# Kernel optimization log

Measured on AMD Instinct MI355X. Metric: run time of the kernel, lower is better.

The kernel has to match this reference:

```python
import jax, jax.numpy as jnp
import numpy as np

# Model dims (from init_kwargs): T=12, dx=4, du=2 -> D = T*(dx+du) = 72
T, DX, DU = 12, 4, 2
D = T * (DX + DU)          # flow_dim = 72
MID = D // 2               # mid-split mask: first MID features transformed
CTX = 2 * DX               # context = cat(start, goal) = 8
HID = 64                   # ResidualNet / MLP hidden size
NBLK = 16                  # number of (LULinear, Coupling) blocks
B = 65536


def setup_inputs() -> dict:
    key = jax.random.key(0)
    ks = jax.random.split(key, 16)
    n = lambda k, s, sc=1.0: sc * jax.random.normal(k, s, dtype=jnp.float32)
    inp = {
        "trajectories": n(ks[0], (B, T, DX + DU)),
        "start": n(ks[1], (B, DX)),
        "goal": n(ks[2], (B, DX)),
        # LULinear params per block: strictly-lower / strictly-upper entries,
        # unconstrained diag (softplus(0.5413)~=1 -> near-identity init), bias
        "lu_lower": n(ks[3], (NBLK, D, D), 0.01),
        "lu_upper": n(ks[4], (NBLK, D, D), 0.01),
        "lu_diag": 0.5413 + n(ks[5], (NBLK, D), 0.01),
        "lu_bias": n(ks[6], (NBLK, D), 0.01),
        # Coupling conditioner ResidualNet (in=MID+CTX, hidden=64, 2 blocks, out=2*MID)
        "cn_W0": n(ks[7], (NBLK, HID, MID + CTX), 0.05),
        "cn_b0": jnp.zeros((NBLK, HID), jnp.float32),
        "cn_ctxW": n(ks[8], (NBLK, 2, HID, CTX), 0.1),
        "cn_ctxb": jnp.zeros((NBLK, 2, HID), jnp.float32),
        "cn_l1W": n(ks[9], (NBLK, 2, HID, HID), 0.1),
        "cn_l1b": jnp.zeros((NBLK, 2, HID), jnp.float32),
        "cn_l2W": n(ks[10], (NBLK, 2, HID, HID), 0.1),
        "cn_l2b": jnp.zeros((NBLK, 2, HID), jnp.float32),
        "cn_Wf": n(ks[11], (NBLK, D, HID), 0.05),
        "cn_bf": jnp.zeros((NBLK, D), jnp.float32),
        # ConditionalDiagonalNormal context encoder MLP: ctx -> 2*D
        "enc_W1": n(ks[12], (HID, CTX), 0.1),
        "enc_b1": jnp.zeros((HID,), jnp.float32),
        "enc_W2": n(ks[13], (2 * D, HID), 0.05),
        "enc_b2": jnp.zeros((2 * D,), jnp.float32),
    }
    return inp


def reference(trajectories, start, goal, lu_lower, lu_upper, lu_diag, lu_bias,
              cn_W0, cn_b0, cn_ctxW, cn_ctxb, cn_l1W, cn_l1b, cn_l2W, cn_l2b,
              cn_Wf, cn_bf, enc_W1, enc_b1, enc_W2, enc_b2):
    Bn = trajectories.shape[0]
    x = trajectories.reshape(Bn, D)
    ctx = jnp.concatenate([start, goal], axis=1)  # [B, CTX]
    eye = jnp.eye(D, dtype=x.dtype)

    def resnet(h, W0, b0, cW, cb, l1W, l1b, l2W, l2b, Wf, bf):
        # nflows ResidualNet: initial layer on cat(inputs, context), 2 residual
        # blocks with GLU context gating, final linear.
        t = jnp.concatenate([h, ctx], axis=1) @ W0.T + b0
        for i in range(2):
            a = jax.nn.relu(t) @ l1W[i].T + l1b[i]
            a = jax.nn.relu(a) @ l2W[i].T + l2b[i]
            t = t + a * jax.nn.sigmoid(ctx @ cW[i].T + cb[i])  # GLU
        return t @ Wf.T + bf

    def body(carry, p):
        x, ld = carry
        lL, lU, ldg, lb, W0, b0, cW, cb, l1W, l1b, l2W, l2b, Wf, bf = p
        # LULinear: W = L @ U, L unit lower-tri, U upper-tri, diag = softplus + eps
        diag = jax.nn.softplus(ldg) + 1e-3
        W = (jnp.tril(lL, -1) + eye) @ (jnp.triu(lU, 1) + jnp.diag(diag))
        x = x @ W.T + lb
        ld = ld + jnp.sum(jnp.log(diag))
        # Affine coupling, mid-split: first MID transformed, last MID identity
        h_id = x[:, MID:]
        params = resnet(h_id, W0, b0, cW, cb, l1W, l1b, l2W, l2b, Wf, bf)
        shift = params[:, :MID]
        scale = jax.nn.sigmoid(params[:, MID:] + 2.0) + 1e-3
        x = jnp.concatenate([x[:, :MID] * scale + shift, h_id], axis=1)
        ld = ld + jnp.sum(jnp.log(scale), axis=1)
        return (x, ld), None

    stacked = (lu_lower, lu_upper, lu_diag, lu_bias, cn_W0, cn_b0, cn_ctxW,
               cn_ctxb, cn_l1W, cn_l1b, cn_l2W, cn_l2b, cn_Wf, cn_bf)
    (noise, logdet), _ = jax.lax.scan(body, (x, jnp.zeros((Bn,), x.dtype)), stacked)

    # ConditionalDiagonalNormal base: encoder MLP ctx -> (means, log_stds)
    h = jax.nn.relu(ctx @ enc_W1.T + enc_b1)
    p = h @ enc_W2.T + enc_b2
    means, log_std = p[:, :D], p[:, D:]
    z = (noise - means) * jnp.exp(-log_std)
    base_lp = (-0.5 * jnp.sum(z * z, axis=1) - jnp.sum(log_std, axis=1)
               - 0.5 * D * jnp.log(2.0 * jnp.pi))
    return base_lp + logdet
```

## Files before the change

kernel.cpp:

```cpp
#include <hip/hip_runtime.h>
#include <math.h>

#define DD   72
#define MID  36
#define NBLK 16

typedef _Float16 half8 __attribute__((ext_vector_type(8)));
typedef _Float16 half4 __attribute__((ext_vector_type(4)));
typedef float    f32x4 __attribute__((ext_vector_type(4)));

#define PB    37376
#define S1O   0
#define S2O   7680
#define RBO   11776
#define RB_L1 0
#define RB_L2 4096
#define RB_GW 8192
#define S4O   32256
#define E1O   (16 * PB)
#define E2O   (E1O + 2048)

__device__ inline half4 pk4(f32x4 v) {
    half4 h; h[0] = (_Float16)v[0]; h[1] = (_Float16)v[1];
    h[2] = (_Float16)v[2]; h[3] = (_Float16)v[3]; return h;
}
__device__ inline half4 pk4r(f32x4 v) {
    half4 h;
    h[0] = (_Float16)fmaxf(v[0], 0.f); h[1] = (_Float16)fmaxf(v[1], 0.f);
    h[2] = (_Float16)fmaxf(v[2], 0.f); h[3] = (_Float16)fmaxf(v[3], 0.f);
    return h;
}
__device__ inline float sigf(float x) {
    return __fdividef(1.f, 1.f + __expf(-x));
}
__device__ inline f32x4 MF(half8 a, half8 b, f32x4 c) {
    return __builtin_amdgcn_mfma_f32_16x16x32_f16(a, b, c, 0, 0, 0);
}

__global__ __launch_bounds__(256) void prep_all(
    const float* __restrict__ lu_lower, const float* __restrict__ lu_upper,
    const float* __restrict__ lu_diag,  const float* __restrict__ lu_bias,
    const float* __restrict__ cn_W0, const float* __restrict__ cn_ctxW,
    const float* __restrict__ cn_l1W, const float* __restrict__ cn_l2W,
    const float* __restrict__ cn_Wf, const float* __restrict__ enc_W1,
    const float* __restrict__ enc_W2,
    const float* __restrict__ cn_b0, const float* __restrict__ cn_ctxb,
    const float* __restrict__ enc_b1,
    _Float16* __restrict__ AR, float* __restrict__ wsLd)
{
    const int tid = threadIdx.x;
    __shared__ float Ls[DD][DD + 1];
    __shared__ float Us[DD][DD + 1];
    __shared__ float diag[DD], ldp[DD];

    if (blockIdx.x < 80) {
        const int wg  = blockIdx.x;
        const int blk = wg / 5, mt = wg % 5;
        const float* L = lu_lower + blk * DD * DD;
        const float* U = lu_upper + blk * DD * DD;
        for (int e = tid; e < DD * DD; e += 256) {
            Ls[e / DD][e % DD] = L[e];
            Us[e / DD][e % DD] = U[e];
        }
        if (tid < DD) {
            float v  = lu_diag[blk * DD + tid];
            float sp = log1pf(expf(v)) + 0.001f;
            diag[tid] = sp; ldp[tid] = logf(sp);
        }
        __syncthreads();
        if (mt == 0 && tid == 0) {
            float s = 0.f;
            for (int i = 0; i < DD; ++i) s += ldp[i];
            wsLd[blk] = s;
        }
        if (tid < 192) {
            const int kt = tid >> 6, lane = tid & 63;
            const int m  = mt * 16 + (lane & 15);
            const int k0 = kt * 32 + (lane >> 4) * 8;
            float acc[8] = {0.f,0.f,0.f,0.f,0.f,0.f,0.f,0.f};
            if (m < DD) {
                for (int kk = 0; kk < m; ++kk) {
                    const float a = Ls[m][kk];
                    #pragma unroll
                    for (int j = 0; j < 8; ++j) {
                        const int k = k0 + j;
                        if (k < DD && kk < k) acc[j] = fmaf(a, Us[kk][k], acc[j]);
                    }
                }
                #pragma unroll
                for (int j = 0; j < 8; ++j) {
                    const int k = k0 + j;
                    if (k < DD) {
                        if      (m < k)  acc[j] += Us[m][k];
                        else if (m == k) acc[j] += diag[k];
                        else             acc[j] += Ls[m][k] * diag[k];
                    }
                }
            }
            half8 hv;
            #pragma unroll
            for (int j = 0; j < 8; ++j) {
                const int k = k0 + j;
                float v = 0.f;
                if (m < DD) {
                    if      (k < DD)  v = acc[j];
                    else if (k == DD) v = lu_bias[blk * DD + m];
                }
                hv[j] = (_Float16)v;
            }
            *(half8*)(AR + (size_t)blk * PB + S1O + (size_t)(mt * 3 + kt) * 512
                      + (size_t)lane * 8) = hv;
        }
        return;
    }

    int gid = (blockIdx.x - 80) * 256 + tid;
    int fid = gid >> 6, lane = gid & 63;
    if (fid >= 950) return;
    const int mrow = lane & 15, kcol0 = (lane >> 4) * 8;

    const float* src = nullptr; const float* bias = nullptr;
    size_t dst = 0;
    int m = 0, kbase = 0, rows = 64, kv_lo = 0, kv_hi = 64, sstr = 64, ksub = 0, kbias = -1;

    if (fid < 128) {
        int blk = fid >> 3, f = fid & 7;
        int mt = f >> 1, kt = f & 1;
        src = cn_W0 + (size_t)blk * 64 * 44; sstr = 44;
        dst = (size_t)blk * PB + S2O + (size_t)f * 512;
        m = mt * 16 + mrow; kbase = kt * 32 + kcol0; kv_hi = 44;
        bias = cn_b0 + (size_t)blk * 64; kbias = 44;
    } else if (fid < 384) {
        int id = fid - 128, bi = id >> 3, f = id & 7;
        int mt = f >> 1, kt = f & 1;
        src = cn_l1W + (size_t)bi * 4096;
        dst = (size_t)(bi >> 1) * PB + RBO + (size_t)(bi & 1) * 10240 + RB_L1 + (size_t)f * 512;
        m = mt * 16 + mrow; kbase = kt * 32 + kcol0;
    } else if (fid < 640) {
        int id = fid - 384, bi = id >> 3, f = id & 7;
        int mt = f >> 1, kt = f & 1;
        src = cn_l2W + (size_t)bi * 4096;
        dst = (size_t)(bi >> 1) * PB + RBO + (size_t)(bi & 1) * 10240 + RB_L2 + (size_t)f * 512;
        m = mt * 16 + mrow; kbase = kt * 32 + kcol0;
    } else if (fid < 768) {
        int id = fid - 640, bi = id >> 2, mt = id & 3;
        src = cn_ctxW + (size_t)bi * 512; sstr = 8;
        dst = (size_t)(bi >> 1) * PB + RBO + (size_t)(bi & 1) * 10240 + RB_GW + (size_t)mt * 512;
        m = mt * 16 + mrow; kbase = 32 + kcol0; kv_lo = 36; kv_hi = 44; ksub = 36;
        bias = cn_ctxb + (size_t)bi * 64; kbias = 44;
    } else if (fid < 928) {
        int id = fid - 768, blk = id / 10, f = id % 10;
        int mt = f >> 1, kt = f & 1;
        src = cn_Wf + (size_t)blk * 4608;
        dst = (size_t)blk * PB + S4O + (size_t)f * 512;
        m = mt * 16 + mrow; kbase = kt * 32 + kcol0; rows = 72;
    } else if (fid < 932) {
        int mt = fid - 928;
        src = enc_W1; sstr = 8;
        dst = E1O + (size_t)mt * 512;
        m = mt * 16 + mrow; kbase = 32 + kcol0; kv_lo = 36; kv_hi = 44; ksub = 36;
        bias = enc_b1; kbias = 44;
    } else {
        int id = fid - 932, mt = id >> 1, kt = id & 1;
        src = enc_W2;
        dst = E2O + (size_t)id * 512;
        m = mt * 16 + mrow; kbase = kt * 32 + kcol0; rows = 144;
    }
    half8 hv;
    #pragma unroll
    for (int j = 0; j < 8; ++j) {
        const int k = kbase + j;
        float v = 0.f;
        if (m < rows) {
            if (k >= kv_lo && k < kv_hi) v = src[(size_t)m * sstr + (k - ksub)];
            else if (k == kbias)         v = bias[m];
        }
        hv[j] = (_Float16)v;
    }
    *(half8*)(AR + dst + (size_t)lane * 8) = hv;
}

#define LDH8(off) (*(const half8*)(AR + (size_t)(off) + lane8))
#define MFMA_A(acc, off, bf) acc = MF(LDH8(off), bf, acc)

__global__ __launch_bounds__(256, 4) void flow_kernel(
    const float* __restrict__ traj,
    const float* __restrict__ start,
    const float* __restrict__ goal,
    const float* __restrict__ cn_l1b,
    const float* __restrict__ cn_l2b,
    const float* __restrict__ cn_bf,
    const float* __restrict__ enc_b2,
    const _Float16* __restrict__ AR,
    const float* __restrict__ wsLd,
    float* __restrict__ out, int B)
{
    __shared__ __align__(16) _Float16 ActX[64 * 104];
    __shared__ __align__(16) _Float16 ActH[64 * 72];
    __shared__ __align__(16) _Float16 ActT[64 * 72];

    const int tid  = threadIdx.x;
    const int lane = tid & 63;
    const int w    = __builtin_amdgcn_readfirstlane(tid >> 6);
    const int n    = lane & 15, lg = lane >> 4;
    const int bg0  = blockIdx.x * 64;
    const size_t lane8 = (size_t)lane * 8;

    #pragma unroll
    for (int r = 0; r < 9; ++r) {
        int e = tid + 256 * r;
        int b = e / 36, p = e % 36;
        float2 v = *(const float2*)(traj + (size_t)(bg0 + b) * DD + 2 * p);
        ActX[b * 104 + 2 * p]     = (_Float16)v.x;
        ActX[b * 104 + 2 * p + 1] = (_Float16)v.y;
    }
    #pragma unroll
    for (int r = 0; r < 8; ++r) {
        int e = tid + 256 * r;
        int b = e / 32, c = 72 + e % 32;
        ActX[b * 104 + c] = (c == 72) ? (_Float16)1.f : (_Float16)0.f;
    }
    {
        int b = tid >> 2, cp = tid & 3;
        const float* s = (cp < 2) ? (start + (size_t)(bg0 + b) * 4 + 2 * cp)
                                  : (goal  + (size_t)(bg0 + b) * 4 + 2 * (cp - 2));
        ActH[b * 72 + 36 + 2 * cp]     = (_Float16)s[0];
        ActH[b * 72 + 36 + 2 * cp + 1] = (_Float16)s[1];
    }
    #pragma unroll
    for (int r = 0; r < 7; ++r) {
        int e = tid + 256 * r;
        int b = e / 28, c = 44 + e % 28;
        ActH[b * 72 + c] = (c == 44) ? (_Float16)1.f : (_Float16)0.f;
    }

    half8 s1p0 = LDH8(S1O + 0 * 512), s1p1 = LDH8(S1O + 1 * 512),
          s1p2 = LDH8(S1O + 2 * 512), s1p3 = LDH8(S1O + 3 * 512),
          s1p4 = LDH8(S1O + 4 * 512), s1p5 = LDH8(S1O + 5 * 512);

    __syncthreads();

    const int bx = (16 * w + n) * 104;
    const int bh = (16 * w + n) * 72;
    const int bt = (16 * w + n) * 72;

    float ld_acc = 0.f;
    const f32x4 z4 = {0.f, 0.f, 0.f, 0.f};

    #pragma unroll 1
    for (int blk = 0; blk < NBLK; ++blk) {
        __syncthreads();
        const size_t B0 = (size_t)blk * PB;

        half8 f6  = LDH8(B0 + S1O + 6 * 512),  f7  = LDH8(B0 + S1O + 7 * 512),
              f8  = LDH8(B0 + S1O + 8 * 512),  f9  = LDH8(B0 + S1O + 9 * 512),
              f10 = LDH8(B0 + S1O + 10 * 512), f11 = LDH8(B0 + S1O + 11 * 512),
              f12 = LDH8(B0 + S1O + 12 * 512), f13 = LDH8(B0 + S1O + 13 * 512),
              f14 = LDH8(B0 + S1O + 14 * 512);
        half8 bx0 = *(const half8*)&ActX[bx + 0  + lg * 8];
        half8 bx1 = *(const half8*)&ActX[bx + 32 + lg * 8];
        half8 bx2 = *(const half8*)&ActX[bx + 64 + lg * 8];
        f32x4 y[5];
        y[0] = MF(s1p2, bx2, MF(s1p1, bx1, MF(s1p0, bx0, z4)));
        y[1] = MF(s1p5, bx2, MF(s1p4, bx1, MF(s1p3, bx0, z4)));
        y[2] = MF(f8,  bx2, MF(f7,  bx1, MF(f6,  bx0, z4)));
        y[3] = MF(f11, bx2, MF(f10, bx1, MF(f9,  bx0, z4)));
        y[4] = MF(f14, bx2, MF(f13, bx1, MF(f12, bx0, z4)));

        half8 g0 = LDH8(B0 + S2O + 0 * 512), g1 = LDH8(B0 + S2O + 1 * 512),
              g2 = LDH8(B0 + S2O + 2 * 512), g3 = LDH8(B0 + S2O + 3 * 512),
              g4 = LDH8(B0 + S2O + 4 * 512), g5 = LDH8(B0 + S2O + 5 * 512),
              g6 = LDH8(B0 + S2O + 6 * 512), g7 = LDH8(B0 + S2O + 7 * 512);
        if (lg >= 1) { half4 hv = pk4(y[2]); int m0 = 32 + lg * 4;
            *(half4*)&ActX[bx + m0] = hv; *(half4*)&ActH[bh + m0 - 36] = hv; }
        {            half4 hv = pk4(y[3]); int m0 = 48 + lg * 4;
            *(half4*)&ActX[bx + m0] = hv; *(half4*)&ActH[bh + m0 - 36] = hv; }
        if (lg < 2) { half4 hv = pk4(y[4]); int m0 = 64 + lg * 4;
            *(half4*)&ActX[bx + m0] = hv; *(half4*)&ActH[bh + m0 - 36] = hv; }
        half8 bh0 = *(const half8*)&ActH[bh + 0  + lg * 8];
        half8 bh1 = *(const half8*)&ActH[bh + 32 + lg * 8];
        f32x4 t[4];
        t[0] = MF(g1, bh1, MF(g0, bh0, z4));
        t[1] = MF(g3, bh1, MF(g2, bh0, z4));
        t[2] = MF(g5, bh1, MF(g4, bh0, z4));
        t[3] = MF(g7, bh1, MF(g6, bh0, z4));

        #pragma unroll
        for (int i = 0; i < 2; ++i) {
            const size_t RB = B0 + RBO + (size_t)i * 10240;
            half8 r0 = LDH8(RB + RB_L1 + 0 * 512), r1 = LDH8(RB + RB_L1 + 1 * 512),
                  r2 = LDH8(RB + RB_L1 + 2 * 512), r3 = LDH8(RB + RB_L1 + 3 * 512),
                  r4 = LDH8(RB + RB_L1 + 4 * 512), r5 = LDH8(RB + RB_L1 + 5 * 512),
                  r6 = LDH8(RB + RB_L1 + 6 * 512), r7 = LDH8(RB + RB_L1 + 7 * 512);
            #pragma unroll
            for (int mt = 0; mt < 4; ++mt)
                *(half4*)&ActT[bt + mt * 16 + lg * 4] = pk4r(t[mt]);
            half8 bt0 = *(const half8*)&ActT[bt + 0  + lg * 8];
            half8 bt1 = *(const half8*)&ActT[bt + 32 + lg * 8];
            f32x4 a1[4];
            a1[0] = MF(r1, bt1, MF(r0, bt0, z4));
            a1[1] = MF(r3, bt1, MF(r2, bt0, z4));
            a1[2] = MF(r5, bt1, MF(r4, bt0, z4));
            a1[3] = MF(r7, bt1, MF(r6, bt0, z4));
            half8 q0 = LDH8(RB + RB_L2 + 0 * 512), q1 = LDH8(RB + RB_L2 + 1 * 512),
                  q2 = LDH8(RB + RB_L2 + 2 * 512), q3 = LDH8(RB + RB_L2 + 3 * 512),
                  q4 = LDH8(RB + RB_L2 + 4 * 512), q5 = LDH8(RB + RB_L2 + 5 * 512),
                  q6 = LDH8(RB + RB_L2 + 6 * 512), q7 = LDH8(RB + RB_L2 + 7 * 512);
            half8 w0 = LDH8(RB + RB_GW + 0 * 512), w1 = LDH8(RB + RB_GW + 1 * 512),
                  w2 = LDH8(RB + RB_GW + 2 * 512), w3 = LDH8(RB + RB_GW + 3 * 512);
            #pragma unroll
            for (int mt = 0; mt < 4; ++mt) {
                const float4 bb = *(const float4*)(cn_l1b + (blk * 2 + i) * 64 + mt * 16 + lg * 4);
                a1[mt][0] += bb.x; a1[mt][1] += bb.y; a1[mt][2] += bb.z; a1[mt][3] += bb.w;
                *(half4*)&ActT[bt + mt * 16 + lg * 4] = pk4r(a1[mt]);
            }
            bt0 = *(const half8*)&ActT[bt + 0  + lg * 8];
            bt1 = *(const half8*)&ActT[bt + 32 + lg * 8];
            f32x4 a2[4], gg[4];
            a2[0] = MF(q1, bt1, MF(q0, bt0, z4));
            a2[1] = MF(q3, bt1, MF(q2, bt0, z4));
            a2[2] = MF(q5, bt1, MF(q4, bt0, z4));
            a2[3] = MF(q7, bt1, MF(q6, bt0, z4));
            gg[0] = MF(w0, bh1, z4); gg[1] = MF(w1, bh1, z4);
            gg[2] = MF(w2, bh1, z4); gg[3] = MF(w3, bh1, z4);
            #pragma unroll
            for (int mt = 0; mt < 4; ++mt) {
                const float4 b2 = *(const float4*)(cn_l2b + (blk * 2 + i) * 64 + mt * 16 + lg * 4);
                #pragma unroll
                for (int r = 0; r < 4; ++r) {
                    float av = a2[mt][r] + ((const float*)&b2)[r];
                    t[mt][r] = fmaf(av, sigf(gg[mt][r]), t[mt][r]);
                }
            }
        }

        half8 h0 = LDH8(B0 + S4O + 0 * 512), h1 = LDH8(B0 + S4O + 1 * 512),
              h2 = LDH8(B0 + S4O + 2 * 512), h3 = LDH8(B0 + S4O + 3 * 512),
              h4 = LDH8(B0 + S4O + 4 * 512), h5 = LDH8(B0 + S4O + 5 * 512),
              h6 = LDH8(B0 + S4O + 6 * 512), h7 = LDH8(B0 + S4O + 7 * 512),
              h8 = LDH8(B0 + S4O + 8 * 512), h9 = LDH8(B0 + S4O + 9 * 512);
        #pragma unroll
        for (int mt = 0; mt < 4; ++mt)
            *(half4*)&ActT[bt + mt * 16 + lg * 4] = pk4(t[mt]);
        half8 bt0 = *(const half8*)&ActT[bt + 0  + lg * 8];
        half8 bt1 = *(const half8*)&ActT[bt + 32 + lg * 8];
        f32x4 p[5];
        p[0] = MF(h1, bt1, MF(h0, bt0, z4));
        p[1] = MF(h3, bt1, MF(h2, bt0, z4));
        p[2] = MF(h5, bt1, MF(h4, bt0, z4));
        p[3] = MF(h7, bt1, MF(h6, bt0, z4));
        p[4] = MF(h9, bt1, MF(h8, bt0, z4));
        #pragma unroll
        for (int mt = 0; mt < 5; ++mt) {
            int bm = mt * 16 + lg * 4; if (bm > 68) bm = 68;
            const float4 bb = *(const float4*)(cn_bf + blk * DD + bm);
            p[mt][0] += bb.x; p[mt][1] += bb.y; p[mt][2] += bb.z; p[mt][3] += bb.w;
        }

        {
            const size_t Bn = (size_t)(blk < NBLK - 1 ? blk + 1 : blk) * PB;
            s1p0 = LDH8(Bn + S1O + 0 * 512); s1p1 = LDH8(Bn + S1O + 1 * 512);
            s1p2 = LDH8(Bn + S1O + 2 * 512); s1p3 = LDH8(Bn + S1O + 3 * 512);
            s1p4 = LDH8(Bn + S1O + 4 * 512); s1p5 = LDH8(Bn + S1O + 5 * 512);
        }

        if (lg >= 1) {
            f32x4 s;
            #pragma unroll
            for (int r = 0; r < 4; ++r) {
                s[r] = sigf(p[2][r] + 2.f) + 0.001f;
                ld_acc += __logf(s[r]);
            }
            *(half4*)&ActT[bt + (32 + lg * 4) - 36] = pk4(s);
        }
        {
            f32x4 s;
            #pragma unroll
            for (int r = 0; r < 4; ++r) {
                s[r] = sigf(p[3][r] + 2.f) + 0.001f;
                ld_acc += __logf(s[r]);
            }
            *(half4*)&ActT[bt + (48 + lg * 4) - 36] = pk4(s);
        }
        if (lg < 2) {
            f32x4 s;
            #pragma unroll
            for (int r = 0; r < 4; ++r) {
                s[r] = sigf(p[4][r] + 2.f) + 0.001f;
                ld_acc += __logf(s[r]);
            }
            *(half4*)&ActT[bt + (64 + lg * 4) - 36] = pk4(s);
        }
        {
            half4 sv = *(const half4*)&ActT[bt + lg * 4];
            f32x4 xn;
            #pragma unroll
            for (int r = 0; r < 4; ++r) xn[r] = fmaf(y[0][r], (float)sv[r], p[0][r]);
            *(half4*)&ActX[bx + lg * 4] = pk4(xn);
        }
        {
            half4 sv = *(const half4*)&ActT[bt + 16 + lg * 4];
            f32x4 xn;
            #pragma unroll
            for (int r = 0; r < 4; ++r) xn[r] = fmaf(y[1][r], (float)sv[r], p[1][r]);
            *(half4*)&ActX[bx + 16 + lg * 4] = pk4(xn);
        }
        if (lg == 0) {
            half4 sv = *(const half4*)&ActT[bt + 32];
            f32x4 xn;
            #pragma unroll
            for (int r = 0; r < 4; ++r) xn[r] = fmaf(y[2][r], (float)sv[r], p[2][r]);
            *(half4*)&ActX[bx + 32] = pk4(xn);
        }
    }

    half8 bh1 = *(const half8*)&ActH[bh + 32 + lg * 8];
    #pragma unroll
    for (int mt = 0; mt < 4; ++mt) {
        f32x4 a = z4;
        MFMA_A(a, E1O + mt * 512, bh1);
        *(half4*)&ActT[bt + mt * 16 + lg * 4] = pk4r(a);
    }
    half8 bt0 = *(const half8*)&ActT[bt + 0  + lg * 8];
    half8 bt1 = *(const half8*)&ActT[bt + 32 + lg * 8];
    f32x4 me[9];
    #pragma unroll
    for (int mt = 0; mt < 9; ++mt) {
        f32x4 a = z4;
        MFMA_A(a, E2O + (mt * 2 + 0) * 512, bt0);
        MFMA_A(a, E2O + (mt * 2 + 1) * 512, bt1);
        const float4 bb = *(const float4*)(enc_b2 + mt * 16 + lg * 4);
        me[mt][0] = a[0] + bb.x; me[mt][1] = a[1] + bb.y;
        me[mt][2] = a[2] + bb.z; me[mt][3] = a[3] + bb.w;
    }
    float slsp = 0.f, qp = 0.f;
    if (lg >= 2) {
        #pragma unroll
        for (int r = 0; r < 4; ++r) slsp += me[4][r];
        *(half4*)&ActT[bt + lg * 4 - 8] = pk4(me[4]);
    }
    #pragma unroll
    for (int mt = 5; mt < 9; ++mt) {
        #pragma unroll
        for (int r = 0; r < 4; ++r) slsp += me[mt][r];
        *(half4*)&ActT[bt + (mt * 16 + lg * 4) - 72] = pk4(me[mt]);
    }
    #pragma unroll
    for (int mt = 0; mt < 4; ++mt) {
        int m0 = mt * 16 + lg * 4;
        half4 xv = *(const half4*)&ActX[bx + m0];
        half4 lv = *(const half4*)&ActT[bt + m0];
        #pragma unroll
        for (int r = 0; r < 4; ++r) {
            float zz = ((float)xv[r] - me[mt][r]) * __expf(-(float)lv[r]);
            qp = fmaf(zz, zz, qp);
        }
    }
    if (lg < 2) {
        int m0 = 64 + lg * 4;
        half4 xv = *(const half4*)&ActX[bx + m0];
        half4 lv = *(const half4*)&ActT[bt + m0];
        #pragma unroll
        for (int r = 0; r < 4; ++r) {
            float zz = ((float)xv[r] - me[4][r]) * __expf(-(float)lv[r]);
            qp = fmaf(zz, zz, qp);
        }
    }

    qp     += __shfl_xor(qp, 16);     qp     += __shfl_xor(qp, 32);
    slsp   += __shfl_xor(slsp, 16);   slsp   += __shfl_xor(slsp, 32);
    ld_acc += __shfl_xor(ld_acc, 16); ld_acc += __shfl_xor(ld_acc, 32);
    if (lane < 16) {
        float ldsum = 0.f;
        #pragma unroll
        for (int k = 0; k < NBLK; ++k) ldsum += wsLd[k];
        out[bg0 + 16 * w + lane] = -0.5f * qp - slsp - 66.1635744f + ld_acc + ldsum;
    }
}

extern "C" void kernel_launch(void* const* d_in, const int* in_sizes, int n_in,
                              void* d_out, int out_size, void* d_ws, size_t ws_size,
                              hipStream_t stream) {
    const float* traj     = (const float*)d_in[0];
    const float* start    = (const float*)d_in[1];
    const float* goal     = (const float*)d_in[2];
    const float* lu_lower = (const float*)d_in[3];
    const float* lu_upper = (const float*)d_in[4];
    const float* lu_diag  = (const float*)d_in[5];
    const float* lu_bias  = (const float*)d_in[6];
    const float* cn_W0    = (const float*)d_in[7];
    const float* cn_b0    = (const float*)d_in[8];
    const float* cn_ctxW  = (const float*)d_in[9];
    const float* cn_ctxb  = (const float*)d_in[10];
    const float* cn_l1W   = (const float*)d_in[11];
    const float* cn_l1b   = (const float*)d_in[12];
    const float* cn_l2W   = (const float*)d_in[13];
    const float* cn_l2b   = (const float*)d_in[14];
    const float* cn_Wf    = (const float*)d_in[15];
    const float* cn_bf    = (const float*)d_in[16];
    const float* enc_W1   = (const float*)d_in[17];
    const float* enc_b1   = (const float*)d_in[18];
    const float* enc_W2   = (const float*)d_in[19];
    const float* enc_b2   = (const float*)d_in[20];

    float* outp = (float*)d_out;
    const int B = in_sizes[0] / DD;

    float*     wsLd = (float*)d_ws;
    _Float16*  AR   = (_Float16*)((char*)d_ws + 256);

    hipLaunchKernelGGL(prep_all, dim3(80 + 238), dim3(256), 0, stream,
                       lu_lower, lu_upper, lu_diag, lu_bias,
                       cn_W0, cn_ctxW, cn_l1W, cn_l2W, cn_Wf, enc_W1, enc_W2,
                       cn_b0, cn_ctxb, enc_b1, AR, wsLd);

    hipLaunchKernelGGL(flow_kernel, dim3(B / 64), dim3(256), 0, stream,
                       traj, start, goal,
                       cn_l1b, cn_l2b, cn_bf, enc_b2,
                       AR, wsLd, outp, B);
}
```

Before: 354.3 us.

## Process two 64-row tiles per block to reuse weight fragments across tiles

Each block now handles 128 batch rows as two 64-row sub-tiles, so every weight fragment loaded from global memory into registers feeds MFMAs for both sub-tiles. This halves the per-row weight-load traffic and the number of per-block barriers, and gives more independent MFMA chains to interleave. In exchange, LDS and register use per block roughly double, launch bounds drop to 2 blocks per SM, and the grid halves, which lowers occupancy and may cause register spilling.

```diff
diff --git a/kernel.cpp b/kernel.cpp
--- a/kernel.cpp
+++ b/kernel.cpp
@@ -19,6 +19,9 @@
 #define S4O   32256
 #define E1O   (16 * PB)
 #define E2O   (E1O + 2048)
+
+#define XOFF  (64 * 104)
+#define HOFF  (64 * 72)
 
 __device__ inline half4 pk4(f32x4 v) {
     half4 h; h[0] = (_Float16)v[0]; h[1] = (_Float16)v[1];
@@ -183,7 +186,7 @@
 #define LDH8(off) (*(const half8*)(AR + (size_t)(off) + lane8))
 #define MFMA_A(acc, off, bf) acc = MF(LDH8(off), bf, acc)
 
-__global__ __launch_bounds__(256, 4) void flow_kernel(
+__global__ __launch_bounds__(256, 2) void flow_kernel(
     const float* __restrict__ traj,
     const float* __restrict__ start,
     const float* __restrict__ goal,
@@ -195,19 +198,19 @@
     const float* __restrict__ wsLd,
     float* __restrict__ out, int B)
 {
-    __shared__ __align__(16) _Float16 ActX[64 * 104];
-    __shared__ __align__(16) _Float16 ActH[64 * 72];
-    __shared__ __align__(16) _Float16 ActT[64 * 72];
+    __shared__ __align__(16) _Float16 ActX[128 * 104];
+    __shared__ __align__(16) _Float16 ActH[128 * 72];
+    __shared__ __align__(16) _Float16 ActT[128 * 72];
 
     const int tid  = threadIdx.x;
     const int lane = tid & 63;
     const int w    = __builtin_amdgcn_readfirstlane(tid >> 6);
     const int n    = lane & 15, lg = lane >> 4;
-    const int bg0  = blockIdx.x * 64;
+    const int bg0  = blockIdx.x * 128;
     const size_t lane8 = (size_t)lane * 8;
 
     #pragma unroll
-    for (int r = 0; r < 9; ++r) {
+    for (int r = 0; r < 18; ++r) {
         int e = tid + 256 * r;
         int b = e / 36, p = e % 36;
         float2 v = *(const float2*)(traj + (size_t)(bg0 + b) * DD + 2 * p);
@@ -215,20 +218,22 @@
         ActX[b * 104 + 2 * p + 1] = (_Float16)v.y;
     }
     #pragma unroll
-    for (int r = 0; r < 8; ++r) {
+    for (int r = 0; r < 16; ++r) {
         int e = tid + 256 * r;
         int b = e / 32, c = 72 + e % 32;
         ActX[b * 104 + c] = (c == 72) ? (_Float16)1.f : (_Float16)0.f;
     }
-    {
-        int b = tid >> 2, cp = tid & 3;
+    #pragma unroll
+    for (int r = 0; r < 2; ++r) {
+        int e = tid + 256 * r;
+        int b = e >> 2, cp = e & 3;
         const float* s = (cp < 2) ? (start + (size_t)(bg0 + b) * 4 + 2 * cp)
                                   : (goal  + (size_t)(bg0 + b) * 4 + 2 * (cp - 2));
         ActH[b * 72 + 36 + 2 * cp]     = (_Float16)s[0];
         ActH[b * 72 + 36 + 2 * cp + 1] = (_Float16)s[1];
     }
     #pragma unroll
-    for (int r = 0; r < 7; ++r) {
+    for (int r = 0; r < 14; ++r) {
         int e = tid + 256 * r;
         int b = e / 28, c = 44 + e % 28;
         ActH[b * 72 + c] = (c == 44) ? (_Float16)1.f : (_Float16)0.f;
@@ -242,9 +247,8 @@
 
     const int bx = (16 * w + n) * 104;
     const int bh = (16 * w + n) * 72;
-    const int bt = (16 * w + n) * 72;
-
-    float ld_acc = 0.f;
+
+    float ldac[2] = {0.f, 0.f};
     const f32x4 z4 = {0.f, 0.f, 0.f, 0.f};
 
     #pragma unroll 1
@@ -257,33 +261,46 @@
               f10 = LDH8(B0 + S1O + 10 * 512), f11 = LDH8(B0 + S1O + 11 * 512),
               f12 = LDH8(B0 + S1O + 12 * 512), f13 = LDH8(B0 + S1O + 13 * 512),
               f14 = LDH8(B0 + S1O + 14 * 512);
-        half8 bx0 = *(const half8*)&ActX[bx + 0  + lg * 8];
-        half8 bx1 = *(const half8*)&ActX[bx + 32 + lg * 8];
-        half8 bx2 = *(const half8*)&ActX[bx + 64 + lg * 8];
-        f32x4 y[5];
-        y[0] = MF(s1p2, bx2, MF(s1p1, bx1, MF(s1p0, bx0, z4)));
-        y[1] = MF(s1p5, bx2, MF(s1p4, bx1, MF(s1p3, bx0, z4)));
-        y[2] = MF(f8,  bx2, MF(f7,  bx1, MF(f6,  bx0, z4)));
-        y[3] = MF(f11, bx2, MF(f10, bx1, MF(f9,  bx0, z4)));
-        y[4] = MF(f14, bx2, MF(f13, bx1, MF(f12, bx0, z4)));
+        f32x4 y[2][5];
+        #pragma unroll
+        for (int u = 0; u < 2; ++u) {
+            const int ox = bx + u * XOFF;
+            half8 b0v = *(const half8*)&ActX[ox + 0  + lg * 8];
+            half8 b1v = *(const half8*)&ActX[ox + 32 + lg * 8];
+            half8 b2v = *(const half8*)&ActX[ox + 64 + lg * 8];
+            y[u][0] = MF(s1p2, b2v, MF(s1p1, b1v, MF(s1p0, b0v, z4)));
+            y[u][1] = MF(s1p5, b2v, MF(s1p4, b1v, MF(s1p3, b0v, z4)));
+            y[u][2] = MF(f8,  b2v, MF(f7,  b1v, MF(f6,  b0v, z4)));
+            y[u][3] = MF(f11, b2v, MF(f10, b1v, MF(f9,  b0v, z4)));
+            y[u][4] = MF(f14, b2v, MF(f13, b1v, MF(f12, b0v, z4)));
+        }
 
         half8 g0 = LDH8(B0 + S2O + 0 * 512), g1 = LDH8(B0 + S2O + 1 * 512),
               g2 = LDH8(B0 + S2O + 2 * 512), g3 = LDH8(B0 + S2O + 3 * 512),
               g4 = LDH8(B0 + S2O + 4 * 512), g5 = LDH8(B0 + S2O + 5 * 512),
               g6 = LDH8(B0 + S2O + 6 * 512), g7 = LDH8(B0 + S2O + 7 * 512);
-        if (lg >= 1) { half4 hv = pk4(y[2]); int m0 = 32 + lg * 4;
-            *(half4*)&ActX[bx + m0] = hv; *(half4*)&ActH[bh + m0 - 36] = hv; }
-        {            half4 hv = pk4(y[3]); int m0 = 48 + lg * 4;
-            *(half4*)&ActX[bx + m0] = hv; *(half4*)&ActH[bh + m0 - 36] = hv; }
-        if (lg < 2) { half4 hv = pk4(y[4]); int m0 = 64 + lg * 4;
-            *(half4*)&ActX[bx + m0] = hv; *(half4*)&ActH[bh + m0 - 36] = hv; }
-        half8 bh0 = *(const half8*)&ActH[bh + 0  + lg * 8];
-        half8 bh1 = *(const half8*)&ActH[bh + 32 + lg * 8];
-        f32x4 t[4];
-        t[0] = MF(g1, bh1, MF(g0, bh0, z4));
-        t[1] = MF(g3, bh1, MF(g2, bh0, z4));
-        t[2] = MF(g5, bh1, MF(g4, bh0, z4));
-        t[3] = MF(g7, bh1, MF(g6, bh0, z4));
+        #pragma unroll
+        for (int u = 0; u < 2; ++u) {
+            const int ox = bx + u * XOFF, oh = bh + u * HOFF;
+            if (lg >= 1) { half4 hv = pk4(y[u][2]); int m0 = 32 + lg * 4;
+                *(half4*)&ActX[ox + m0] = hv; *(half4*)&ActH[oh + m0 - 36] = hv; }
+            {            half4 hv = pk4(y[u][3]); int m0 = 48 + lg * 4;
+                *(half4*)&ActX[ox + m0] = hv; *(half4*)&ActH[oh + m0 - 36] = hv; }
+            if (lg < 2) { half4 hv = pk4(y[u][4]); int m0 = 64 + lg * 4;
+                *(half4*)&ActX[ox + m0] = hv; *(half4*)&ActH[oh + m0 - 36] = hv; }
+        }
+        half8 bhv0[2], bhv1[2];
+        f32x4 t[2][4];
+        #pragma unroll
+        for (int u = 0; u < 2; ++u) {
+            const int oh = bh + u * HOFF;
+            bhv0[u] = *(const half8*)&ActH[oh + 0  + lg * 8];
+            bhv1[u] = *(const half8*)&ActH[oh + 32 + lg * 8];
+            t[u][0] = MF(g1, bhv1[u], MF(g0, bhv0[u], z4));
+            t[u][1] = MF(g3, bhv1[u], MF(g2, bhv0[u], z4));
+            t[u][2] = MF(g5, bhv1[u], MF(g4, bhv0[u], z4));
+            t[u][3] = MF(g7, bhv1[u], MF(g6, bhv0[u], z4));
+        }
 
         #pragma unroll
         for (int i = 0; i < 2; ++i) {
@@ -293,43 +310,66 @@
                   r4 = LDH8(RB + RB_L1 + 4 * 512), r5 = LDH8(RB + RB_L1 + 5 * 512),
                   r6 = LDH8(RB + RB_L1 + 6 * 512), r7 = LDH8(RB + RB_L1 + 7 * 512);
             #pragma unroll
-            for (int mt = 0; mt < 4; ++mt)
-                *(half4*)&ActT[bt + mt * 16 + lg * 4] = pk4r(t[mt]);
-            half8 bt0 = *(const half8*)&ActT[bt + 0  + lg * 8];
-            half8 bt1 = *(const half8*)&ActT[bt + 32 + lg * 8];
-            f32x4 a1[4];
-            a1[0] = MF(r1, bt1, MF(r0, bt0, z4));
-            a1[1] = MF(r3, bt1, MF(r2, bt0, z4));
-            a1[2] = MF(r5, bt1, MF(r4, bt0, z4));
-            a1[3] = MF(r7, bt1, MF(r6, bt0, z4));
+            for (int u = 0; u < 2; ++u) {
+                const int ot = bh + u * HOFF;
+                #pragma unroll
+                for (int mt = 0; mt < 4; ++mt)
+                    *(half4*)&ActT[ot + mt * 16 + lg * 4] = pk4r(t[u][mt]);
+            }
+            f32x4 a1[2][4];
+            #pragma unroll
+            for (int u = 0; u < 2; ++u) {
+                const int ot = bh + u * HOFF;
+                half8 c0 = *(const half8*)&ActT[ot + 0  + lg * 8];
+                half8 c1 = *(const half8*)&ActT[ot + 32 + lg * 8];
+                a1[u][0] = MF(r1, c1, MF(r0, c0, z4));
+                a1[u][1] = MF(r3, c1, MF(r2, c0, z4));
+                a1[u][2] = MF(r5, c1, MF(r4, c0, z4));
+                a1[u][3] = MF(r7, c1, MF(r6, c0, z4));
+            }
             half8 q0 = LDH8(RB + RB_L2 + 0 * 512), q1 = LDH8(RB + RB_L2 + 1 * 512),
                   q2 = LDH8(RB + RB_L2 + 2 * 512), q3 = LDH8(RB + RB_L2 + 3 * 512),
                   q4 = LDH8(RB + RB_L2 + 4 * 512), q5 = LDH8(RB + RB_L2 + 5 * 512),
                   q6 = LDH8(RB + RB_L2 + 6 * 512), q7 = LDH8(RB + RB_L2 + 7 * 512);
             half8 w0 = LDH8(RB + RB_GW + 0 * 512), w1 = LDH8(RB + RB_GW + 1 * 512),
                   w2 = LDH8(RB + RB_GW + 2 * 512), w3 = LDH8(RB + RB_GW + 3 * 512);
-            #pragma unroll
-            for (int mt = 0; mt < 4; ++mt) {
-                const float4 bb = *(const float4*)(cn_l1b + (blk * 2 + i) * 64 + mt * 16 + lg * 4);
-                a1[mt][0] += bb.x; a1[mt][1] += bb.y; a1[mt][2] += bb.z; a1[mt][3] += bb.w;
-                *(half4*)&ActT[bt + mt * 16 + lg * 4] = pk4r(a1[mt]);
-            }
-            bt0 = *(const half8*)&ActT[bt + 0  + lg * 8];
-            bt1 = *(const half8*)&ActT[bt + 32 + lg * 8];
-            f32x4 a2[4], gg[4];
-            a2[0] = MF(q1, bt1, MF(q0, bt0, z4));
-            a2[1] = MF(q3, bt1, MF(q2, bt0, z4));
-            a2[2] = MF(q5, bt1, MF(q4, bt0, z4));
-            a2[3] = MF(q7, bt1, MF(q6, bt0, z4));
-            gg[0] = MF(w0, bh1, z4); gg[1] = MF(w1, bh1, z4);
-            gg[2] = MF(w2, bh1, z4); gg[3] = MF(w3, bh1, z4);
-            #pragma unroll
-            for (int mt = 0; mt < 4; ++mt) {
-                const float4 b2 = *(const float4*)(cn_l2b + (blk * 2 + i) * 64 + mt * 16 + lg * 4);
-                #pragma unroll
-                for (int r = 0; r < 4; ++r) {
-                    float av = a2[mt][r] + ((const float*)&b2)[r];
-                    t[mt][r] = fmaf(av, sigf(gg[mt][r]), t[mt][r]);
+            float4 bb1[4];
+            #pragma unroll
+            for (int mt = 0; mt < 4; ++mt)
+                bb1[mt] = *(const float4*)(cn_l1b + (blk * 2 + i) * 64 + mt * 16 + lg * 4);
+            #pragma unroll
+            for (int u = 0; u < 2; ++u) {
+                const int ot = bh + u * HOFF;
+                #pragma unroll
+                for (int mt = 0; mt < 4; ++mt) {
+                    a1[u][mt][0] += bb1[mt].x; a1[u][mt][1] += bb1[mt].y;
+                    a1[u][mt][2] += bb1[mt].z; a1[u][mt][3] += bb1[mt].w;
+                    *(half4*)&ActT[ot + mt * 16 + lg * 4] = pk4r(a1[u][mt]);
+                }
+            }
+            float4 bb2[4];
+            #pragma unroll
+            for (int mt = 0; mt < 4; ++mt)
+                bb2[mt] = *(const float4*)(cn_l2b + (blk * 2 + i) * 64 + mt * 16 + lg * 4);
+            #pragma unroll
+            for (int u = 0; u < 2; ++u) {
+                const int ot = bh + u * HOFF;
+                half8 c0 = *(const half8*)&ActT[ot + 0  + lg * 8];
+                half8 c1 = *(const half8*)&ActT[ot + 32 + lg * 8];
+                f32x4 a2[4], gg[4];
+                a2[0] = MF(q1, c1, MF(q0, c0, z4));
+                a2[1] = MF(q3, c1, MF(q2, c0, z4));
+                a2[2] = MF(q5, c1, MF(q4, c0, z4));
+                a2[3] = MF(q7, c1, MF(q6, c0, z4));
+                gg[0] = MF(w0, bhv1[u], z4); gg[1] = MF(w1, bhv1[u], z4);
+                gg[2] = MF(w2, bhv1[u], z4); gg[3] = MF(w3, bhv1[u], z4);
+                #pragma unroll
+                for (int mt = 0; mt < 4; ++mt) {
+                    #pragma unroll
+                    for (int r = 0; r < 4; ++r) {
+                        float av = a2[mt][r] + ((const float*)&bb2[mt])[r];
+                        t[u][mt][r] = fmaf(av, sigf(gg[mt][r]), t[u][mt][r]);
+                    }
                 }
             }
         }
@@ -340,21 +380,34 @@
               h6 = LDH8(B0 + S4O + 6 * 512), h7 = LDH8(B0 + S4O + 7 * 512),
               h8 = LDH8(B0 + S4O + 8 * 512), h9 = LDH8(B0 + S4O + 9 * 512);
         #pragma unroll
-        for (int mt = 0; mt < 4; ++mt)
-            *(half4*)&ActT[bt + mt * 16 + lg * 4] = pk4(t[mt]);
-        half8 bt0 = *(const half8*)&ActT[bt + 0  + lg * 8];
-        half8 bt1 = *(const half8*)&ActT[bt + 32 + lg * 8];
-        f32x4 p[5];
-        p[0] = MF(h1, bt1, MF(h0, bt0, z4));
-        p[1] = MF(h3, bt1, MF(h2, bt0, z4));
-        p[2] = MF(h5, bt1, MF(h4, bt0, z4));
-        p[3] = MF(h7, bt1, MF(h6, bt0, z4));
-        p[4] = MF(h9, bt1, MF(h8, bt0, z4));
+        for (int u = 0; u < 2; ++u) {
+            const int ot = bh + u * HOFF;
+            #pragma unroll
+            for (int mt = 0; mt < 4; ++mt)
+                *(half4*)&ActT[ot + mt * 16 + lg * 4] = pk4(t[u][mt]);
+        }
+        float4 bfv[5];
         #pragma unroll
         for (int mt = 0; mt < 5; ++mt) {
             int bm = mt * 16 + lg * 4; if (bm > 68) bm = 68;
-            const float4 bb = *(const float4*)(cn_bf + blk * DD + bm);
-            p[mt][0] += bb.x; p[mt][1] += bb.y; p[mt][2] += bb.z; p[mt][3] += bb.w;
+            bfv[mt] = *(const float4*)(cn_bf + blk * DD + bm);
+        }
+        f32x4 p[2][5];
+        #pragma unroll
+        for (int u = 0; u < 2; ++u) {
+            const int ot = bh + u * HOFF;
+            half8 c0 = *(const half8*)&ActT[ot + 0  + lg * 8];
+            half8 c1 = *(const half8*)&ActT[ot + 32 + lg * 8];
+            p[u][0] = MF(h1, c1, MF(h0, c0, z4));
+            p[u][1] = MF(h3, c1, MF(h2, c0, z4));
+            p[u][2] = MF(h5, c1, MF(h4, c0, z4));
+            p[u][3] = MF(h7, c1, MF(h6, c0, z4));
+            p[u][4] = MF(h9, c1, MF(h8, c0, z4));
+            #pragma unroll
+            for (int mt = 0; mt < 5; ++mt) {
+                p[u][mt][0] += bfv[mt].x; p[u][mt][1] += bfv[mt].y;
+                p[u][mt][2] += bfv[mt].z; p[u][mt][3] += bfv[mt].w;
+            }
         }
 
         {
@@ -364,117 +417,129 @@
             s1p4 = LDH8(Bn + S1O + 4 * 512); s1p5 = LDH8(Bn + S1O + 5 * 512);
         }
 
-        if (lg >= 1) {
-            f32x4 s;
+        #pragma unroll
+        for (int u = 0; u < 2; ++u) {
+            const int ot = bh + u * HOFF, ox = bx + u * XOFF;
+            if (lg >= 1) {
+                f32x4 s;
+                #pragma unroll
+                for (int r = 0; r < 4; ++r) {
+                    s[r] = sigf(p[u][2][r] + 2.f) + 0.001f;
+                    ldac[u] += __logf(s[r]);
+                }
+                *(half4*)&ActT[ot + (32 + lg * 4) - 36] = pk4(s);
+            }
+            {
+                f32x4 s;
+                #pragma unroll
+                for (int r = 0; r < 4; ++r) {
+                    s[r] = sigf(p[u][3][r] + 2.f) + 0.001f;
+                    ldac[u] += __logf(s[r]);
+                }
+                *(half4*)&ActT[ot + (48 + lg * 4) - 36] = pk4(s);
+            }
+            if (lg < 2) {
+                f32x4 s;
+                #pragma unroll
+                for (int r = 0; r < 4; ++r) {
+                    s[r] = sigf(p[u][4][r] + 2.f) + 0.001f;
+                    ldac[u] += __logf(s[r]);
+                }
+                *(half4*)&ActT[ot + (64 + lg * 4) - 36] = pk4(s);
+            }
+            {
+                half4 sv = *(const half4*)&ActT[ot + lg * 4];
+                f32x4 xn;
+                #pragma unroll
+                for (int r = 0; r < 4; ++r) xn[r] = fmaf(y[u][0][r], (float)sv[r], p[u][0][r]);
+                *(half4*)&ActX[ox + lg * 4] = pk4(xn);
+            }
+            {
+                half4 sv = *(const half4*)&ActT[ot + 16 + lg * 4];
+                f32x4 xn;
+                #pragma unroll
+                for (int r = 0; r < 4; ++r) xn[r] = fmaf(y[u][1][r], (float)sv[r], p[u][1][r]);
+                *(half4*)&ActX[ox + 16 + lg * 4] = pk4(xn);
+            }
+            if (lg == 0) {
+                half4 sv = *(const half4*)&ActT[ot + 32];
+                f32x4 xn;
+                #pragma unroll
+                for (int r = 0; r < 4; ++r) xn[r] = fmaf(y[u][2][r], (float)sv[r], p[u][2][r]);
+                *(half4*)&ActX[ox + 32] = pk4(xn);
+            }
+        }
+    }
+
+    float qp[2] = {0.f, 0.f}, slsp[2] = {0.f, 0.f};
+    #pragma unroll
+    for (int u = 0; u < 2; ++u) {
+        const int ot = bh + u * HOFF, ox = bx + u * XOFF, oh = bh + u * HOFF;
+        half8 bh1u = *(const half8*)&ActH[oh + 32 + lg * 8];
+        #pragma unroll
+        for (int mt = 0; mt < 4; ++mt) {
+            f32x4 a = z4;
+            MFMA_A(a, E1O + mt * 512, bh1u);
+            *(half4*)&ActT[ot + mt * 16 + lg * 4] = pk4r(a);
+        }
+        half8 c0 = *(const half8*)&ActT[ot + 0  + lg * 8];
+        half8 c1 = *(const half8*)&ActT[ot + 32 + lg * 8];
+        f32x4 me[9];
+        #pragma unroll
+        for (int mt = 0; mt < 9; ++mt) {
+            f32x4 a = z4;
+            MFMA_A(a, E2O + (mt * 2 + 0) * 512, c0);
+            MFMA_A(a, E2O + (mt * 2 + 1) * 512, c1);
+            const float4 bb = *(const float4*)(enc_b2 + mt * 16 + lg * 4);
+            me[mt][0] = a[0] + bb.x; me[mt][1] = a[1] + bb.y;
+            me[mt][2] = a[2] + bb.z; me[mt][3] = a[3] + bb.w;
+        }
+        if (lg >= 2) {
+            #pragma unroll
+            for (int r = 0; r < 4; ++r) slsp[u] += me[4][r];
+            *(half4*)&ActT[ot + lg * 4 - 8] = pk4(me[4]);
+        }
+        #pragma unroll
+        for (int mt = 5; mt < 9; ++mt) {
+            #pragma unroll
+            for (int r = 0; r < 4; ++r) slsp[u] += me[mt][r];
+            *(half4*)&ActT[ot + (mt * 16 + lg * 4) - 72] = pk4(me[mt]);
+        }
+        #pragma unroll
+        for (int mt = 0; mt < 4; ++mt) {
+            int m0 = mt * 16 + lg * 4;
+            half4 xv = *(const half4*)&ActX[ox + m0];
+            half4 lv = *(const half4*)&ActT[ot + m0];
             #pragma unroll
             for (int r = 0; r < 4; ++r) {
-                s[r] = sigf(p[2][r] + 2.f) + 0.001f;
-                ld_acc += __logf(s[r]);
-            }
-            *(half4*)&ActT[bt + (32 + lg * 4) - 36] = pk4(s);
-        }
-        {
-            f32x4 s;
+                float zz = ((float)xv[r] - me[mt][r]) * __expf(-(float)lv[r]);
+                qp[u] = fmaf(zz, zz, qp[u]);
+            }
+        }
+        if (lg < 2) {
+            int m0 = 64 + lg * 4;
+            half4 xv = *(const half4*)&ActX[ox + m0];
+            half4 lv = *(const half4*)&ActT[ot + m0];
             #pragma unroll
             for (int r = 0; r < 4; ++r) {
-                s[r] = sigf(p[3][r] + 2.f) + 0.001f;
-                ld_acc += __logf(s[r]);
-            }
-            *(half4*)&ActT[bt + (48 + lg * 4) - 36] = pk4(s);
-        }
-        if (lg < 2) {
-            f32x4 s;
-            #pragma unroll
-            for (int r = 0; r < 4; ++r) {
-                s[r] = sigf(p[4][r] + 2.f) + 0.001f;
-                ld_acc += __logf(s[r]);
-            }
-            *(half4*)&ActT[bt + (64 + lg * 4) - 36] = pk4(s);
-        }
-        {
-            half4 sv = *(const half4*)&ActT[bt + lg * 4];
-            f32x4 xn;
-            #pragma unroll
-            for (int r = 0; r < 4; ++r) xn[r] = fmaf(y[0][r], (float)sv[r], p[0][r]);
-            *(half4*)&ActX[bx + lg * 4] = pk4(xn);
-        }
-        {
-            half4 sv = *(const half4*)&ActT[bt + 16 + lg * 4];
-            f32x4 xn;
-            #pragma unroll
-            for (int r = 0; r < 4; ++r) xn[r] = fmaf(y[1][r], (float)sv[r], p[1][r]);
-            *(half4*)&ActX[bx + 16 + lg * 4] = pk4(xn);
-        }
-        if (lg == 0) {
-            half4 sv = *(const half4*)&ActT[bt + 32];
-            f32x4 xn;
-            #pragma unroll
-            for (int r = 0; r < 4; ++r) xn[r] = fmaf(y[2][r], (float)sv[r], p[2][r]);
-            *(half4*)&ActX[bx + 32] = pk4(xn);
-        }
-    }
-
-    half8 bh1 = *(const half8*)&ActH[bh + 32 + lg * 8];
-    #pragma unroll
-    for (int mt = 0; mt < 4; ++mt) {
-        f32x4 a = z4;
-        MFMA_A(a, E1O + mt * 512, bh1);
-        *(half4*)&ActT[bt + mt * 16 + lg * 4] = pk4r(a);
-    }
-    half8 bt0 = *(const half8*)&ActT[bt + 0  + lg * 8];
-    half8 bt1 = *(const half8*)&ActT[bt + 32 + lg * 8];
-    f32x4 me[9];
-    #pragma unroll
-    for (int mt = 0; mt < 9; ++mt) {
-        f32x4 a = z4;
-        MFMA_A(a, E2O + (mt * 2 + 0) * 512, bt0);
-        MFMA_A(a, E2O + (mt * 2 + 1) * 512, bt1);
-        const float4 bb = *(const float4*)(enc_b2 + mt * 16 + lg * 4);
-        me[mt][0] = a[0] + bb.x; me[mt][1] = a[1] + bb.y;
-        me[mt][2] = a[2] + bb.z; me[mt][3] = a[3] + bb.w;
-    }
-    float slsp = 0.f, qp = 0.f;
-    if (lg >= 2) {
-        #pragma unroll
-        for (int r = 0; r < 4; ++r) slsp += me[4][r];
-        *(half4*)&ActT[bt + lg * 4 - 8] = pk4(me[4]);
-    }
-    #pragma unroll
-    for (int mt = 5; mt < 9; ++mt) {
-        #pragma unroll
-        for (int r = 0; r < 4; ++r) slsp += me[mt][r];
-        *(half4*)&ActT[bt + (mt * 16 + lg * 4) - 72] = pk4(me[mt]);
-    }
-    #pragma unroll
-    for (int mt = 0; mt < 4; ++mt) {
-        int m0 = mt * 16 + lg * 4;
-        half4 xv = *(const half4*)&ActX[bx + m0];
-        half4 lv = *(const half4*)&ActT[bt + m0];
-        #pragma unroll
-        for (int r = 0; r < 4; ++r) {
-            float zz = ((float)xv[r] - me[mt][r]) * __expf(-(float)lv[r]);
-            qp = fmaf(zz, zz, qp);
-        }
-    }
-    if (lg < 2) {
-        int m0 = 64 + lg * 4;
-        half4 xv = *(const half4*)&ActX[bx + m0];
-        half4 lv = *(const half4*)&ActT[bt + m0];
-        #pragma unroll
-        for (int r = 0; r < 4; ++r) {
-            float zz = ((float)xv[r] - me[4][r]) * __expf(-(float)lv[r]);
-            qp = fmaf(zz, zz, qp);
-        }
-    }
-
-    qp     += __shfl_xor(qp, 16);     qp     += __shfl_xor(qp, 32);
-    slsp   += __shfl_xor(slsp, 16);   slsp   += __shfl_xor(slsp, 32);
-    ld_acc += __shfl_xor(ld_acc, 16); ld_acc += __shfl_xor(ld_acc, 32);
-    if (lane < 16) {
-        float ldsum = 0.f;
-        #pragma unroll
-        for (int k = 0; k < NBLK; ++k) ldsum += wsLd[k];
-        out[bg0 + 16 * w + lane] = -0.5f * qp - slsp - 66.1635744f + ld_acc + ldsum;
+                float zz = ((float)xv[r] - me[4][r]) * __expf(-(float)lv[r]);
+                qp[u] = fmaf(zz, zz, qp[u]);
+            }
+        }
+    }
+
+    float ldsum = 0.f;
+    #pragma unroll
+    for (int k = 0; k < NBLK; ++k) ldsum += wsLd[k];
+    #pragma unroll
+    for (int u = 0; u < 2; ++u) {
+        float q = qp[u], s = slsp[u], l = ldac[u];
+        q += __shfl_xor(q, 16); q += __shfl_xor(q, 32);
+        s += __shfl_xor(s, 16); s += __shfl_xor(s, 32);
+        l += __shfl_xor(l, 16); l += __shfl_xor(l, 32);
+        if (lane < 16) {
+            out[bg0 + u * 64 + 16 * w + lane] = -0.5f * q - s - 66.1635744f + l + ldsum;
+        }
     }
 }
 
@@ -514,7 +579,7 @@
                        cn_W0, cn_ctxW, cn_l1W, cn_l2W, cn_Wf, enc_W1, enc_W2,
                        cn_b0, cn_ctxb, enc_b1, AR, wsLd);
 
-    hipLaunchKernelGGL(flow_kernel, dim3(B / 64), dim3(256), 0, stream,
+    hipLaunchKernelGGL(flow_kernel, dim3(B / 128), dim3(256), 0, stream,
                        traj, start, goal,
                        cn_l1b, cn_l2b, cn_bf, enc_b2,
                        AR, wsLd, outp, B);
```

After: 375.0 us. +5.8%, slower.
